# Performance work log

Measured on AMD Instinct MI355X. Metric: run time of the kernel, lower is better.

The kernel has to match this reference:

```python
import jax, jax.numpy as jnp
import numpy as np

N = 50000   # nodes
E = 800000  # directed edges
D = 128     # input_channels


def _kaiming(key, shape):
    fan_in = shape[0]
    return jax.random.normal(key, shape, jnp.float32) * np.float32(np.sqrt(2.0 / fan_in))


def setup_inputs():
    key = jax.random.key(0)
    ks = jax.random.split(key, 8)
    x = jax.random.normal(ks[0], (N, D), jnp.float32)
    edge_index = jax.random.randint(ks[1], (2, E), 0, N, dtype=jnp.int32)
    return {
        "x": x,
        "edge_index": edge_index,
        "W_in": _kaiming(ks[2], (D, D)),      "b_in": jnp.zeros((D,), jnp.float32),
        "W1": _kaiming(ks[3], (D, 2 * D)),    "b1": jnp.zeros((2 * D,), jnp.float32),
        "W2": _kaiming(ks[4], (2 * D, D)),    "b2": jnp.zeros((D,), jnp.float32),
        "W3": _kaiming(ks[5], (D, D // 2)),   "b3": jnp.zeros((D // 2,), jnp.float32),
        "W_out": _kaiming(ks[6], (D // 2, 1)), "b_out": jnp.zeros((1,), jnp.float32),
    }


def _gcn_conv(x, src, dst, W, b, n):
    """PyG GCNConv: add self-loops, symmetric D^-1/2 (A+I) D^-1/2 normalization."""
    h = x @ W  # [n, out]
    loop = jnp.arange(n, dtype=src.dtype)
    s = jnp.concatenate([src, loop])  # message sources (x_j)
    d = jnp.concatenate([dst, loop])  # aggregation targets (x_i)
    deg = jax.ops.segment_sum(jnp.ones_like(d, jnp.float32), d, num_segments=n)
    dis = jnp.where(deg > 0, jax.lax.rsqrt(jnp.maximum(deg, 1.0)), 0.0)
    norm = dis[s] * dis[d]  # [E+n]
    msg = h[s] * norm[:, None]  # gather + scale
    out = jax.ops.segment_sum(msg, d, num_segments=n)  # scatter-add
    return out + b


def reference(x, edge_index, W_in, b_in, W1, b1, W2, b2, W3, b3, W_out, b_out):
    src, dst = edge_index[0], edge_index[1]
    n = x.shape[0]
    lrelu = lambda t: jax.nn.leaky_relu(t, 0.01)
    # dropout in eval mode (identity)
    h = lrelu(x @ W_in + b_in)
    h = lrelu(_gcn_conv(h, src, dst, W1, b1, n))
    h = lrelu(_gcn_conv(h, src, dst, W2, b2, n))
    h = lrelu(_gcn_conv(h, src, dst, W3, b3, n))
    return h @ W_out + b_out  # [n, 1]
```

## Files before the change

### kernel.cpp

```cpp
#include <hip/hip_runtime.h>


#define LRELU(v) ((v) > 0.f ? (v) : 0.01f * (v))

typedef __attribute__((ext_vector_type(8))) _Float16 half8;
typedef __attribute__((ext_vector_type(8))) float float8;
typedef __attribute__((ext_vector_type(4))) float floatx4;

constexpr int CAP = 64;

template <int F>
__device__ __forceinline__ half8 loadB(const float* __restrict__ W, int k0,
                                       int col) {
  half8 h;
#pragma unroll
  for (int j = 0; j < 8; ++j) h[j] = (_Float16)W[(long)(k0 + j) * F + col];
  return h;
}

template <int K, int F, int EPI, typename IT>
__device__ __forceinline__ void gemm_tile(const IT* __restrict__ X,
                                          const float* __restrict__ W,
                                          const float* __restrict__ bias,
                                          const int* __restrict__ cnt,
                                          _Float16* __restrict__ out, int M,
                                          int tile, _Float16* __restrict__ xs) {
  constexpr int TM = 64;
  constexpr int PAD = 8;
  constexpr int LK = K + PAD;
  constexpr int CW = F / 4;
  constexpr int NT = CW / 16;
  constexpr int NK = K / 32;

  const int m0 = tile * TM;
  const int tid = threadIdx.x;
  const int w = tid >> 6;
  const int lane = tid & 63;
  const int m = lane & 15;
  const int q = lane >> 4;

  half8 breg[NT][NK];
#pragma unroll
  for (int t = 0; t < NT; ++t)
#pragma unroll
    for (int kc = 0; kc < NK; ++kc)
      breg[t][kc] = loadB<F>(W, kc * 32 + q * 8, w * CW + t * 16 + m);

  constexpr int CPR = K / 8;
  for (int idx = tid; idx < TM * CPR; idx += 256) {
    const int row = idx / CPR;
    const int kk = idx % CPR;
    const int g = m0 + row;
    half8 h = (half8)(_Float16)0.f;
    if (g < M) {
      if constexpr (sizeof(IT) == 4) {
        const float4* p = (const float4*)&X[(long)g * K + kk * 8];
        float4 a = p[0], cc = p[1];
        h[0] = (_Float16)a.x; h[1] = (_Float16)a.y;
        h[2] = (_Float16)a.z; h[3] = (_Float16)a.w;
        h[4] = (_Float16)cc.x; h[5] = (_Float16)cc.y;
        h[6] = (_Float16)cc.z; h[7] = (_Float16)cc.w;
      } else {
        h = *(const half8*)&X[(long)g * K + kk * 8];
      }
    }
    *(half8*)&xs[row * LK + kk * 8] = h;
  }
  __syncthreads();

  floatx4 acc[4][NT];
#pragma unroll
  for (int rt = 0; rt < 4; ++rt)
#pragma unroll
    for (int t = 0; t < NT; ++t) acc[rt][t] = (floatx4){0.f, 0.f, 0.f, 0.f};

#pragma unroll
  for (int kc = 0; kc < NK; ++kc) {
    half8 af[4];
#pragma unroll
    for (int rt = 0; rt < 4; ++rt)
      af[rt] = *(const half8*)&xs[(rt * 16 + m) * LK + kc * 32 + q * 8];
#pragma unroll
    for (int rt = 0; rt < 4; ++rt)
#pragma unroll
      for (int t = 0; t < NT; ++t)
        acc[rt][t] = __builtin_amdgcn_mfma_f32_16x16x32_f16(af[rt], breg[t][kc],
                                                            acc[rt][t], 0, 0, 0);
  }

#pragma unroll
  for (int rt = 0; rt < 4; ++rt) {
#pragma unroll
    for (int r = 0; r < 4; ++r) {
      const int row = m0 + rt * 16 + q * 4 + r;
      if (row < M) {
        float dv = 1.f;
        if constexpr (EPI == 2) dv = rsqrtf((float)cnt[row] + 1.0f);
#pragma unroll
        for (int t = 0; t < NT; ++t) {
          const int col = w * CW + t * 16 + m;
          float v = acc[rt][t][r];
          if constexpr (EPI == 1) { v += bias[col]; v = LRELU(v); }
          if constexpr (EPI == 2) { v *= dv; }
          out[(long)row * F + col] = (_Float16)v;
        }
      }
    }
  }
}

__global__ __launch_bounds__(256) void k_sg(const float* __restrict__ x,
                                            const float* __restrict__ W_in,
                                            const float* __restrict__ b_in,
                                            const int* __restrict__ src,
                                            const int* __restrict__ dst,
                                            int* __restrict__ cnt,
                                            unsigned short* __restrict__ pad,
                                            _Float16* __restrict__ h0,
                                            int N, int E, int PR, int nGroups,
                                            int gemmTiles) {
  __shared__ _Float16 xs[64 * 136];
  const int b = blockIdx.x;
  const int g = b >> 4;
  const int r = b & 15;
  if (r < 8) {
    const int lo = r * PR;
    const int tid = threadIdx.x;
    if ((E & 3) == 0) {
      const int nCh = E >> 10;
      for (int ch = g; ch < nCh; ch += nGroups) {
        const int e0 = ch * 1024 + tid * 4;
        const int4 d4 = *(const int4*)&dst[e0];
        const int4 s4 = *(const int4*)&src[e0];
#pragma unroll
        for (int k = 0; k < 4; ++k) {
          const int d = (&d4.x)[k];
          if ((unsigned)(d - lo) < (unsigned)PR) {
            const int pos = atomicAdd(&cnt[d], 1);
            if (pos < CAP) pad[(long)d * CAP + pos] = (unsigned short)(&s4.x)[k];
          }
        }
      }
      if (g == 0) {
        for (int e = (nCh << 10) + tid; e < E; e += 256) {
          const int d = dst[e];
          if ((unsigned)(d - lo) < (unsigned)PR) {
            const int pos = atomicAdd(&cnt[d], 1);
            if (pos < CAP) pad[(long)d * CAP + pos] = (unsigned short)src[e];
          }
        }
      }
    } else {
      const int nCh = (E + 255) >> 8;
      for (int ch = g; ch < nCh; ch += nGroups) {
        const int e = ch * 256 + tid;
        if (e < E) {
          const int d = dst[e];
          if ((unsigned)(d - lo) < (unsigned)PR) {
            const int pos = atomicAdd(&cnt[d], 1);
            if (pos < CAP) pad[(long)d * CAP + pos] = (unsigned short)src[e];
          }
        }
      }
    }
  } else {
    const int tile = g * 8 + (r - 8);
    if (tile < gemmTiles)
      gemm_tile<128, 128, 1, float>(x, W_in, b_in, nullptr, h0, N, tile, xs);
  }
}

__global__ __launch_bounds__(256) void k_gemm3(const _Float16* __restrict__ X,
                                               const float* __restrict__ W3,
                                               const int* __restrict__ cnt,
                                               _Float16* __restrict__ out,
                                               int M) {
  __shared__ _Float16 xs[64 * 136];
  gemm_tile<128, 64, 2, _Float16>(X, W3, nullptr, cnt, out, M, blockIdx.x, xs);
}

__global__ __launch_bounds__(256) void k_g2x(const _Float16* __restrict__ X,
                                             const float* __restrict__ W1,
                                             const float* __restrict__ b1,
                                             const float* __restrict__ W2,
                                             const int* __restrict__ cnt,
                                             _Float16* __restrict__ out, int M) {
  constexpr int LK1 = 128 + 8;
  constexpr int LK2 = 256 + 8;
  __shared__ _Float16 smem[64 * LK2];
  _Float16* xs = smem;
  _Float16* ys = smem;

  const int m0 = blockIdx.x * 64;
  const int tid = threadIdx.x;
  const int w = tid >> 6;
  const int lane = tid & 63;
  const int m = lane & 15;
  const int q = lane >> 4;

  for (int idx = tid; idx < 64 * 16; idx += 256) {
    const int row = idx >> 4;
    const int kk = idx & 15;
    const int g = m0 + row;
    half8 h = (half8)(_Float16)0.f;
    if (g < M) h = *(const half8*)&X[(long)g * 128 + kk * 8];
    *(half8*)&xs[row * LK1 + kk * 8] = h;
  }

  half8 breg1[4][4];
#pragma unroll
  for (int t = 0; t < 4; ++t)
#pragma unroll
    for (int kc = 0; kc < 4; ++kc)
      breg1[t][kc] = loadB<256>(W1, kc * 32 + q * 8, w * 64 + t * 16 + m);

  __syncthreads();

  floatx4 acc1[4][4];
#pragma unroll
  for (int rt = 0; rt < 4; ++rt)
#pragma unroll
    for (int t = 0; t < 4; ++t) acc1[rt][t] = (floatx4){0.f, 0.f, 0.f, 0.f};

#pragma unroll
  for (int kc = 0; kc < 4; ++kc) {
    half8 af[4];
#pragma unroll
    for (int rt = 0; rt < 4; ++rt)
      af[rt] = *(const half8*)&xs[(rt * 16 + m) * LK1 + kc * 32 + q * 8];
#pragma unroll
    for (int rt = 0; rt < 4; ++rt)
#pragma unroll
      for (int t = 0; t < 4; ++t)
        acc1[rt][t] = __builtin_amdgcn_mfma_f32_16x16x32_f16(af[rt], breg1[t][kc],
                                                             acc1[rt][t], 0, 0, 0);
  }

  half8 breg2[2][8];
#pragma unroll
  for (int t = 0; t < 2; ++t)
#pragma unroll
    for (int kc = 0; kc < 8; ++kc)
      breg2[t][kc] = loadB<128>(W2, kc * 32 + q * 8, w * 32 + t * 16 + m);

  __syncthreads();

#pragma unroll
  for (int rt = 0; rt < 4; ++rt) {
#pragma unroll
    for (int r = 0; r < 4; ++r) {
      const int row = rt * 16 + q * 4 + r;
#pragma unroll
      for (int t = 0; t < 4; ++t) {
        const int col = w * 64 + t * 16 + m;
        float v = acc1[rt][t][r] + b1[col];
        ys[row * LK2 + col] = (_Float16)LRELU(v);
      }
    }
  }

  __syncthreads();

  floatx4 acc2[4][2];
#pragma unroll
  for (int rt = 0; rt < 4; ++rt)
#pragma unroll
    for (int t = 0; t < 2; ++t) acc2[rt][t] = (floatx4){0.f, 0.f, 0.f, 0.f};

#pragma unroll
  for (int kc = 0; kc < 8; ++kc) {
    half8 af[4];
#pragma unroll
    for (int rt = 0; rt < 4; ++rt)
      af[rt] = *(const half8*)&ys[(rt * 16 + m) * LK2 + kc * 32 + q * 8];
#pragma unroll
    for (int rt = 0; rt < 4; ++rt)
#pragma unroll
      for (int t = 0; t < 2; ++t)
        acc2[rt][t] = __builtin_amdgcn_mfma_f32_16x16x32_f16(af[rt], breg2[t][kc],
                                                             acc2[rt][t], 0, 0, 0);
  }

#pragma unroll
  for (int rt = 0; rt < 4; ++rt) {
#pragma unroll
    for (int r = 0; r < 4; ++r) {
      const int row = m0 + rt * 16 + q * 4 + r;
      if (row < M) {
        const float dv = rsqrtf((float)cnt[row] + 1.0f);
#pragma unroll
        for (int t = 0; t < 2; ++t) {
          const int col = w * 32 + t * 16 + m;
          out[(long)row * 128 + col] = (_Float16)(acc2[rt][t][r] * dv);
        }
      }
    }
  }
}

__global__ __launch_bounds__(256) void k_agg_pre(const _Float16* __restrict__ G,
                                                 const unsigned short* __restrict__ pad,
                                                 const int* __restrict__ cnt,
                                                 _Float16* __restrict__ out,
                                                 int N, int gHalf) {
  const int b = blockIdx.x;
  const int ph = (b >= gHalf) ? 1 : 0;
  const int blk = b - ph * gHalf;
  const int col0 = ph << 6;

  const int w = threadIdx.x >> 6;
  const int lane = threadIdx.x & 63;
  const int c = lane & 7;
  const int j = lane >> 3;
  const int n = j >> 2;
  const int jj = j & 3;
  int i = blk * 8 + w * 2 + n;
  const bool valid = (i < N);
  if (!valid) i = N - 1;
  const int cni = cnt[i];
  const int cn = min(cni, CAP);
  const float dvi = rsqrtf((float)cni + 1.f);
  const _Float16* gb = G + col0 + c * 8;
  const unsigned short* pl = pad + (long)i * CAP;

  float8 a0 = {0.f, 0.f, 0.f, 0.f, 0.f, 0.f, 0.f, 0.f};
  float8 a1 = a0, a2 = a0, a3 = a0;
  if (jj == 0) {
    float8 f = __builtin_convertvector(*(const half8*)(gb + (long)i * 128), float8);
#pragma unroll
    for (int k = 0; k < 8; ++k) a0[k] = f[k] * dvi;
  }
  int e = jj;
  for (; e + 12 < cn; e += 16) {
    const int s0 = pl[e], s1 = pl[e + 4], s2 = pl[e + 8], s3 = pl[e + 12];
    const float d0 = rsqrtf((float)cnt[s0] + 1.f);
    const float d1 = rsqrtf((float)cnt[s1] + 1.f);
    const float d2 = rsqrtf((float)cnt[s2] + 1.f);
    const float d3 = rsqrtf((float)cnt[s3] + 1.f);
    float8 f0 = __builtin_convertvector(*(const half8*)(gb + (long)s0 * 128), float8);
    float8 f1 = __builtin_convertvector(*(const half8*)(gb + (long)s1 * 128), float8);
    float8 f2 = __builtin_convertvector(*(const half8*)(gb + (long)s2 * 128), float8);
    float8 f3 = __builtin_convertvector(*(const half8*)(gb + (long)s3 * 128), float8);
#pragma unroll
    for (int k = 0; k < 8; ++k) {
      a0[k] += f0[k] * d0;
      a1[k] += f1[k] * d1;
      a2[k] += f2[k] * d2;
      a3[k] += f3[k] * d3;
    }
  }
  for (; e < cn; e += 4) {
    const int s = pl[e];
    const float d = rsqrtf((float)cnt[s] + 1.f);
    float8 f = __builtin_convertvector(*(const half8*)(gb + (long)s * 128), float8);
#pragma unroll
    for (int k = 0; k < 8; ++k) a0[k] += f[k] * d;
  }
#pragma unroll
  for (int k = 0; k < 8; ++k) a0[k] += a1[k] + a2[k] + a3[k];
#pragma unroll
  for (int k = 0; k < 8; ++k) {
    a0[k] += __shfl_xor(a0[k], 8);
    a0[k] += __shfl_xor(a0[k], 16);
  }
  if (valid && jj == 0) {
    half8 hv;
#pragma unroll
    for (int k = 0; k < 8; ++k) hv[k] = (_Float16)(a0[k] * dvi);
    *(half8*)&out[(long)i * 128 + col0 + c * 8] = hv;
  }
}

__global__ __launch_bounds__(256) void k_agg_post(const _Float16* __restrict__ G,
                                                  const unsigned short* __restrict__ pad,
                                                  const int* __restrict__ cnt,
                                                  const float* __restrict__ bias,
                                                  _Float16* __restrict__ out,
                                                  int N, int gHalf) {
  const int b = blockIdx.x;
  const int ph = (b >= gHalf) ? 1 : 0;
  const int blk = b - ph * gHalf;
  const int col0 = ph << 6;

  const int w = threadIdx.x >> 6;
  const int lane = threadIdx.x & 63;
  const int c = lane & 7;
  const int j = lane >> 3;
  const int n = j >> 2;
  const int jj = j & 3;
  int i = blk * 8 + w * 2 + n;
  const bool valid = (i < N);
  if (!valid) i = N - 1;
  const int cni = cnt[i];
  const int cn = min(cni, CAP);
  const float dvi = rsqrtf((float)cni + 1.f);
  const _Float16* gb = G + col0 + c * 8;
  const unsigned short* pl = pad + (long)i * CAP;

  float8 a0 = {0.f, 0.f, 0.f, 0.f, 0.f, 0.f, 0.f, 0.f};
  float8 a1 = a0, a2 = a0, a3 = a0;
  if (jj == 0)
    a0 = __builtin_convertvector(*(const half8*)(gb + (long)i * 128), float8);
  int e = jj;
  for (; e + 12 < cn; e += 16) {
    const int s0 = pl[e], s1 = pl[e + 4], s2 = pl[e + 8], s3 = pl[e + 12];
    a0 += __builtin_convertvector(*(const half8*)(gb + (long)s0 * 128), float8);
    a1 += __builtin_convertvector(*(const half8*)(gb + (long)s1 * 128), float8);
    a2 += __builtin_convertvector(*(const half8*)(gb + (long)s2 * 128), float8);
    a3 += __builtin_convertvector(*(const half8*)(gb + (long)s3 * 128), float8);
  }
  for (; e < cn; e += 4) {
    const int s = pl[e];
    a0 += __builtin_convertvector(*(const half8*)(gb + (long)s * 128), float8);
  }
  a0 += a1 + a2 + a3;
#pragma unroll
  for (int k = 0; k < 8; ++k) {
    a0[k] += __shfl_xor(a0[k], 8);
    a0[k] += __shfl_xor(a0[k], 16);
  }
  if (valid && jj == 0) {
    half8 hv;
#pragma unroll
    for (int k = 0; k < 8; ++k) {
      float v = a0[k] * dvi + bias[col0 + c * 8 + k];
      hv[k] = (_Float16)LRELU(v);
    }
    *(half8*)&out[(long)i * 128 + col0 + c * 8] = hv;
  }
}

__global__ __launch_bounds__(256) void k_agg_final(const _Float16* __restrict__ G,
                                                   const unsigned short* __restrict__ pad,
                                                   const int* __restrict__ cnt,
                                                   const float* __restrict__ b3,
                                                   const float* __restrict__ Wout,
                                                   const float* __restrict__ bout,
                                                   float* __restrict__ out, int N) {
  const int w = threadIdx.x >> 6;
  const int lane = threadIdx.x & 63;
  const int c = lane & 7;
  const int j = lane >> 3;
  const int n = j >> 2;
  const int jj = j & 3;
  int i = blockIdx.x * 8 + w * 2 + n;
  const bool valid = (i < N);
  if (!valid) i = N - 1;
  const int cni = cnt[i];
  const int cn = min(cni, CAP);
  const float dvi = rsqrtf((float)cni + 1.f);
  const _Float16* gb = G + c * 8;
  const unsigned short* pl = pad + (long)i * CAP;

  float8 a0 = {0.f, 0.f, 0.f, 0.f, 0.f, 0.f, 0.f, 0.f};
  float8 a1 = a0;
  if (jj == 0)
    a0 = __builtin_convertvector(*(const half8*)(gb + (long)i * 64), float8);
  int e = jj;
  for (; e + 4 < cn; e += 8) {
    const int s0 = pl[e], s1 = pl[e + 4];
    a0 += __builtin_convertvector(*(const half8*)(gb + (long)s0 * 64), float8);
    a1 += __builtin_convertvector(*(const half8*)(gb + (long)s1 * 64), float8);
  }
  if (e < cn)
    a0 += __builtin_convertvector(*(const half8*)(gb + (long)pl[e] * 64), float8);
  a0 += a1;
#pragma unroll
  for (int k = 0; k < 8; ++k) {
    a0[k] += __shfl_xor(a0[k], 8);
    a0[k] += __shfl_xor(a0[k], 16);
  }
  float p = 0.f;
#pragma unroll
  for (int k = 0; k < 8; ++k) {
    const int col = c * 8 + k;
    float v = a0[k] * dvi + b3[col];
    v = LRELU(v);
    p += v * Wout[col];
  }
  p += __shfl_xor(p, 1);
  p += __shfl_xor(p, 2);
  p += __shfl_xor(p, 4);
  if (valid && jj == 0 && c == 0) out[i] = p + bout[0];
}


extern "C" void kernel_launch(void* const* d_in, const int* in_sizes, int n_in,
                              void* d_out, int out_size, void* d_ws, size_t ws_size,
                              hipStream_t stream) {
  const float* x     = (const float*)d_in[0];
  const int* eidx    = (const int*)d_in[1];
  const float* W_in  = (const float*)d_in[2];
  const float* b_in  = (const float*)d_in[3];
  const float* W1    = (const float*)d_in[4];
  const float* b1    = (const float*)d_in[5];
  const float* W2    = (const float*)d_in[6];
  const float* b2    = (const float*)d_in[7];
  const float* W3    = (const float*)d_in[8];
  const float* b3    = (const float*)d_in[9];
  const float* W_out = (const float*)d_in[10];
  const float* b_out = (const float*)d_in[11];
  float* out = (float*)d_out;

  const int N = in_sizes[0] / 128;
  const int E = in_sizes[1] / 2;
  const int* src = eidx;
  const int* dst = eidx + E;
  const int PR = (N + 7) / 8;

  size_t off = 0;
  char* base = (char*)d_ws;
  auto alloc = [&](size_t bytes) -> void* {
    void* p = base + off;
    off = (off + bytes + 255) & ~(size_t)255;
    return p;
  };
  int* cnt            = (int*)alloc((size_t)N * sizeof(int));
  unsigned short* pad = (unsigned short*)alloc((size_t)N * CAP * 2);
  _Float16* buf1      = (_Float16*)alloc((size_t)N * 128 * 2);
  _Float16* buf2      = (_Float16*)alloc((size_t)N * 128 * 2);
  _Float16* buf3      = (_Float16*)alloc((size_t)N * 64 * 2);

  hipMemsetAsync(cnt, 0, (size_t)N * sizeof(int), stream);

  const int nGroups = 256;
  const int gRows = (N + 63) / 64;
  const int gHalf = (N + 7) / 8;
  const int gAggF = (N + 7) / 8;

  k_sg<<<nGroups * 16, 256, 0, stream>>>(x, W_in, b_in, src, dst, cnt, pad,
                                         buf1, N, E, PR, nGroups, gRows);
  k_agg_pre<<<2 * gHalf, 256, 0, stream>>>(buf1, pad, cnt, buf2, N, gHalf);
  k_g2x<<<gRows, 256, 0, stream>>>(buf2, W1, b1, W2, cnt, buf1, N);
  k_agg_post<<<2 * gHalf, 256, 0, stream>>>(buf1, pad, cnt, b2, buf2, N, gHalf);
  k_gemm3<<<gRows, 256, 0, stream>>>(buf2, W3, cnt, buf3, N);
  k_agg_final<<<gAggF, 256, 0, stream>>>(buf3, pad, cnt, b3, W_out, b_out,
                                         out, N);
}
```

Measured before the change: 286.4 us.

## Split scatter from input GEMM and prescale features by source degree norm

The fused scatter+input-GEMM kernel is split into a plain edge-scatter kernel and a separate input GEMM. The GEMM epilogue now multiplies each row by its D^-1/2 factor, so the first aggregation no longer looks up and rsqrt's the source degree for every edge. The scatter also drops the destination-range partitioning, so each edge is handled by exactly one thread instead of being filtered by eight blocks. The cost is one extra kernel launch and losing the overlap between scatter and GEMM.

```diff
diff --git a/kernel.cpp b/kernel.cpp
--- a/kernel.cpp
+++ b/kernel.cpp
@@ -95,11 +95,12 @@
       const int row = m0 + rt * 16 + q * 4 + r;
       if (row < M) {
         float dv = 1.f;
-        if constexpr (EPI == 2) dv = rsqrtf((float)cnt[row] + 1.0f);
+        if constexpr (EPI == 0 || EPI == 2) dv = rsqrtf((float)cnt[row] + 1.0f);
 #pragma unroll
         for (int t = 0; t < NT; ++t) {
           const int col = w * CW + t * 16 + m;
           float v = acc[rt][t][r];
+          if constexpr (EPI == 0) { v += bias[col]; v = LRELU(v); v *= dv; }
           if constexpr (EPI == 1) { v += bias[col]; v = LRELU(v); }
           if constexpr (EPI == 2) { v *= dv; }
           out[(long)row * F + col] = (_Float16)v;
@@ -109,65 +110,38 @@
   }
 }
 
-__global__ __launch_bounds__(256) void k_sg(const float* __restrict__ x,
-                                            const float* __restrict__ W_in,
-                                            const float* __restrict__ b_in,
-                                            const int* __restrict__ src,
-                                            const int* __restrict__ dst,
-                                            int* __restrict__ cnt,
-                                            unsigned short* __restrict__ pad,
-                                            _Float16* __restrict__ h0,
-                                            int N, int E, int PR, int nGroups,
-                                            int gemmTiles) {
+__global__ __launch_bounds__(256) void k_scat(const int* __restrict__ src,
+                                              const int* __restrict__ dst,
+                                              int* __restrict__ cnt,
+                                              unsigned short* __restrict__ pad,
+                                              int E) {
+  const int e0 = blockIdx.x * 1024 + (int)threadIdx.x * 4;
+  if (e0 + 3 < E) {
+    const int4 d4 = *(const int4*)&dst[e0];
+    const int4 s4 = *(const int4*)&src[e0];
+#pragma unroll
+    for (int k = 0; k < 4; ++k) {
+      const int d = (&d4.x)[k];
+      const int pos = atomicAdd(&cnt[d], 1);
+      if (pos < CAP) pad[(long)d * CAP + pos] = (unsigned short)(&s4.x)[k];
+    }
+  } else {
+    for (int e = e0; e < E; ++e) {
+      const int d = dst[e];
+      const int pos = atomicAdd(&cnt[d], 1);
+      if (pos < CAP) pad[(long)d * CAP + pos] = (unsigned short)src[e];
+    }
+  }
+}
+
+__global__ __launch_bounds__(256) void k_gemm1(const float* __restrict__ X,
+                                               const float* __restrict__ W,
+                                               const float* __restrict__ bias,
+                                               const int* __restrict__ cnt,
+                                               _Float16* __restrict__ out,
+                                               int M) {
   __shared__ _Float16 xs[64 * 136];
-  const int b = blockIdx.x;
-  const int g = b >> 4;
-  const int r = b & 15;
-  if (r < 8) {
-    const int lo = r * PR;
-    const int tid = threadIdx.x;
-    if ((E & 3) == 0) {
-      const int nCh = E >> 10;
-      for (int ch = g; ch < nCh; ch += nGroups) {
-        const int e0 = ch * 1024 + tid * 4;
-        const int4 d4 = *(const int4*)&dst[e0];
-        const int4 s4 = *(const int4*)&src[e0];
-#pragma unroll
-        for (int k = 0; k < 4; ++k) {
-          const int d = (&d4.x)[k];
-          if ((unsigned)(d - lo) < (unsigned)PR) {
-            const int pos = atomicAdd(&cnt[d], 1);
-            if (pos < CAP) pad[(long)d * CAP + pos] = (unsigned short)(&s4.x)[k];
-          }
-        }
-      }
-      if (g == 0) {
-        for (int e = (nCh << 10) + tid; e < E; e += 256) {
-          const int d = dst[e];
-          if ((unsigned)(d - lo) < (unsigned)PR) {
-            const int pos = atomicAdd(&cnt[d], 1);
-            if (pos < CAP) pad[(long)d * CAP + pos] = (unsigned short)src[e];
-          }
-        }
-      }
-    } else {
-      const int nCh = (E + 255) >> 8;
-      for (int ch = g; ch < nCh; ch += nGroups) {
-        const int e = ch * 256 + tid;
-        if (e < E) {
-          const int d = dst[e];
-          if ((unsigned)(d - lo) < (unsigned)PR) {
-            const int pos = atomicAdd(&cnt[d], 1);
-            if (pos < CAP) pad[(long)d * CAP + pos] = (unsigned short)src[e];
-          }
-        }
-      }
-    }
-  } else {
-    const int tile = g * 8 + (r - 8);
-    if (tile < gemmTiles)
-      gemm_tile<128, 128, 1, float>(x, W_in, b_in, nullptr, h0, N, tile, xs);
-  }
+  gemm_tile<128, 128, 0, float>(X, W, bias, cnt, out, M, blockIdx.x, xs);
 }
 
 __global__ __launch_bounds__(256) void k_gemm3(const _Float16* __restrict__ X,
@@ -325,39 +299,21 @@
 
   float8 a0 = {0.f, 0.f, 0.f, 0.f, 0.f, 0.f, 0.f, 0.f};
   float8 a1 = a0, a2 = a0, a3 = a0;
-  if (jj == 0) {
-    float8 f = __builtin_convertvector(*(const half8*)(gb + (long)i * 128), float8);
-#pragma unroll
-    for (int k = 0; k < 8; ++k) a0[k] = f[k] * dvi;
-  }
+  if (jj == 0)
+    a0 = __builtin_convertvector(*(const half8*)(gb + (long)i * 128), float8);
   int e = jj;
   for (; e + 12 < cn; e += 16) {
     const int s0 = pl[e], s1 = pl[e + 4], s2 = pl[e + 8], s3 = pl[e + 12];
-    const float d0 = rsqrtf((float)cnt[s0] + 1.f);
-    const float d1 = rsqrtf((float)cnt[s1] + 1.f);
-    const float d2 = rsqrtf((float)cnt[s2] + 1.f);
-    const float d3 = rsqrtf((float)cnt[s3] + 1.f);
-    float8 f0 = __builtin_convertvector(*(const half8*)(gb + (long)s0 * 128), float8);
-    float8 f1 = __builtin_convertvector(*(const half8*)(gb + (long)s1 * 128), float8);
-    float8 f2 = __builtin_convertvector(*(const half8*)(gb + (long)s2 * 128), float8);
-    float8 f3 = __builtin_convertvector(*(const half8*)(gb + (long)s3 * 128), float8);
-#pragma unroll
-    for (int k = 0; k < 8; ++k) {
-      a0[k] += f0[k] * d0;
-      a1[k] += f1[k] * d1;
-      a2[k] += f2[k] * d2;
-      a3[k] += f3[k] * d3;
-    }
+    a0 += __builtin_convertvector(*(const half8*)(gb + (long)s0 * 128), float8);
+    a1 += __builtin_convertvector(*(const half8*)(gb + (long)s1 * 128), float8);
+    a2 += __builtin_convertvector(*(const half8*)(gb + (long)s2 * 128), float8);
+    a3 += __builtin_convertvector(*(const half8*)(gb + (long)s3 * 128), float8);
   }
   for (; e < cn; e += 4) {
     const int s = pl[e];
-    const float d = rsqrtf((float)cnt[s] + 1.f);
-    float8 f = __builtin_convertvector(*(const half8*)(gb + (long)s * 128), float8);
-#pragma unroll
-    for (int k = 0; k < 8; ++k) a0[k] += f[k] * d;
-  }
-#pragma unroll
-  for (int k = 0; k < 8; ++k) a0[k] += a1[k] + a2[k] + a3[k];
+    a0 += __builtin_convertvector(*(const half8*)(gb + (long)s * 128), float8);
+  }
+  a0 += a1 + a2 + a3;
 #pragma unroll
   for (int k = 0; k < 8; ++k) {
     a0[k] += __shfl_xor(a0[k], 8);
@@ -506,7 +462,6 @@
   const int E = in_sizes[1] / 2;
   const int* src = eidx;
   const int* dst = eidx + E;
-  const int PR = (N + 7) / 8;
 
   size_t off = 0;
   char* base = (char*)d_ws;
@@ -523,13 +478,13 @@
 
   hipMemsetAsync(cnt, 0, (size_t)N * sizeof(int), stream);
 
-  const int nGroups = 256;
+  const int gScat = (E + 1023) / 1024;
   const int gRows = (N + 63) / 64;
   const int gHalf = (N + 7) / 8;
   const int gAggF = (N + 7) / 8;
 
-  k_sg<<<nGroups * 16, 256, 0, stream>>>(x, W_in, b_in, src, dst, cnt, pad,
-                                         buf1, N, E, PR, nGroups, gRows);
+  k_scat<<<gScat, 256, 0, stream>>>(src, dst, cnt, pad, E);
+  k_gemm1<<<gRows, 256, 0, stream>>>(x, W_in, b_in, cnt, buf1, N);
   k_agg_pre<<<2 * gHalf, 256, 0, stream>>>(buf1, pad, cnt, buf2, N, gHalf);
   k_g2x<<<gRows, 256, 0, stream>>>(buf2, W1, b1, W2, cnt, buf1, N);
   k_agg_post<<<2 * gHalf, 256, 0, stream>>>(buf1, pad, cnt, b2, buf2, N, gHalf);
```

Result: slower. 294.0 us (+2.6%).
